# Performance work log

Hardware: AMD Instinct MI355X
Metric: run time of the kernel (lower is better)

The kernel has to match this reference:

```python
import jax, jax.numpy as jnp
import numpy as np

N_EMBED = 1024
EMBED_DIM = 64
BETA = 0.25


def setup_inputs() -> dict:
    key = jax.random.key(0)
    k1, k2 = jax.random.split(key)
    z = jax.random.normal(k1, (16, EMBED_DIM, 64, 64), dtype=jnp.float32)
    # torch init: uniform(-1/n_embed, 1/n_embed)
    embed_weight = jax.random.uniform(
        k2, (N_EMBED, EMBED_DIM), dtype=jnp.float32,
        minval=-1.0 / N_EMBED, maxval=1.0 / N_EMBED)
    return {"z": z, "embed_weight": embed_weight}


def reference(z, embed_weight):
    # z: (B, C, H, W) with C == embed_dim
    n_embed = embed_weight.shape[0]
    zp = jnp.transpose(z, (0, 2, 3, 1))                     # (B,H,W,C)
    zf = zp.reshape(-1, zp.shape[-1])                       # (N,C)
    # squared euclidean distances: ||z||^2 - 2 z.e + ||e||^2
    dist = (jnp.sum(zf * zf, axis=1, keepdims=True)
            - 2.0 * (zf @ embed_weight.T)
            + jnp.sum(embed_weight * embed_weight, axis=1))  # (N,n_embed)
    embed_index = jnp.argmin(dist, axis=1)                  # (N,)
    embed_onehot = jax.nn.one_hot(embed_index, n_embed, dtype=zf.dtype)
    # one-hot @ codebook is just a gather
    quantize = embed_weight[embed_index].reshape(zp.shape)  # (B,H,W,C)
    vq_loss = (jnp.mean((jax.lax.stop_gradient(quantize) - zp) ** 2)
               + BETA * jnp.mean((quantize - jax.lax.stop_gradient(zp)) ** 2))
    # straight-through estimator
    quantize_st = zp + jax.lax.stop_gradient(quantize - zp)
    e_mean = jnp.mean(embed_onehot, axis=0)
    perplexity = jnp.exp(-jnp.sum(e_mean * jnp.log(e_mean + 1e-10)))
    quantize_out = jnp.transpose(quantize_st, (0, 3, 1, 2))  # (B,C,H,W)
    return (quantize_out, vq_loss, perplexity, embed_onehot, embed_index)
```

## Files before the change

### kernel.cpp

```cpp
#include <hip/hip_runtime.h>
#include <math.h>


#define HW 4096
#define OUT_Q    0ull
#define OUT_LOSS 4194304ull
#define OUT_PERP 4194305ull
#define OUT_OH   4194306ull
#define OUT_IDX  71303170ull

typedef float f32x16 __attribute__((ext_vector_type(16)));

__global__ void vq_setup(const float* __restrict__ W,
                         float* __restrict__ wsf, int* __restrict__ wsi) {
    const int b = blockIdx.x, tid = threadIdx.x;
    if (tid < 64) wsi[b * 64 + tid] = 0;
    if (b == 0 && tid == 0) wsf[1024] = 0.0f;
    const int wave = tid >> 6, lane = tid & 63;
    for (int p = 0; p < 16; ++p) {
        const int code = b * 64 + p * 4 + wave;
        const float a = W[code * 64 + lane];
        const float sq = __fmul_rn(a, a);
        float t = sq;
        #pragma unroll
        for (int m = 1; m < 8; ++m) t = __fadd_rn(t, __shfl(sq, lane + 8 * m, 64));
        const float u  = __fadd_rn(t, __shfl_xor(t, 1, 64));
        const float v  = __fadd_rn(u, __shfl_xor(u, 2, 64));
        const float w2 = __fadd_rn(v, __shfl_xor(v, 4, 64));
        if (lane == 0) wsf[1028 + code] = w2;
    }
}

__global__ __launch_bounds__(256, 2)
void vq_main(const float* __restrict__ Z, const float* __restrict__ W,
             float* __restrict__ out, float* __restrict__ wsf, int* __restrict__ wsi) {
    __shared__ __align__(16) float qT[64 * 65];
    __shared__ __align__(16) float ldsC[1024];
    __shared__ float cand_v[256];
    __shared__ int   cand_i[256];
    __shared__ int   mi[64];

    const int tid  = threadIdx.x;
    const int wave = tid >> 6;
    const int lane = tid & 63;
    const int blk  = blockIdx.x;
    const int b    = blk >> 6;
    const int hw0  = (blk & 63) << 6;
    const int rowbase = b * HW + hw0;

    ((float4*)ldsC)[tid] = ((const float4*)(wsf + 1028))[tid];

    const float* zb = Z + (size_t)b * 64 * HW + hw0 + lane;
    float zr[64];
    #pragma unroll
    for (int c = 0; c < 64; ++c) zr[c] = zb[(size_t)c * HW];

    float r[8];
    #pragma unroll
    for (int j = 0; j < 8; ++j) r[j] = __fmul_rn(zr[j], zr[j]);
    #pragma unroll
    for (int i = 8; i < 64; i += 8) {
        #pragma unroll
        for (int j = 0; j < 8; ++j) r[j] = __fadd_rn(r[j], __fmul_rn(zr[i + j], zr[i + j]));
    }
    const float A = __fadd_rn(__fadd_rn(__fadd_rn(r[0], r[1]), __fadd_rn(r[2], r[3])),
                              __fadd_rn(__fadd_rn(r[4], r[5]), __fadd_rn(r[6], r[7])));

    __syncthreads();

    const float* Wwave = (const float*)((const char*)W +
                         __builtin_amdgcn_readfirstlane(wave << 8));

    float bestv = __builtin_huge_valf();
    int   besti = 0;

    for (int i = 0; i < 256; ++i) {
        const int code = i * 4 + wave;
        const float* wrow = (const float*)((const char*)Wwave + (i << 10));
        f32x16 a0, a1, a2, a3;
        asm volatile(
            "s_load_dwordx16 %0, %4, 0x0\n\t"
            "s_load_dwordx16 %1, %4, 0x40\n\t"
            "s_load_dwordx16 %2, %4, 0x80\n\t"
            "s_load_dwordx16 %3, %4, 0xc0\n\t"
            "s_waitcnt lgkmcnt(0)"
            : "=&s"(a0), "=&s"(a1), "=&s"(a2), "=&s"(a3)
            : "s"(wrow));
        float dot = 0.0f;
        #pragma unroll
        for (int k = 0; k < 16; ++k) dot = __fmaf_rn(zr[k],      a0[k], dot);
        #pragma unroll
        for (int k = 0; k < 16; ++k) dot = __fmaf_rn(zr[16 + k], a1[k], dot);
        #pragma unroll
        for (int k = 0; k < 16; ++k) dot = __fmaf_rn(zr[32 + k], a2[k], dot);
        #pragma unroll
        for (int k = 0; k < 16; ++k) dot = __fmaf_rn(zr[48 + k], a3[k], dot);
        const float d = __fadd_rn(__fsub_rn(A, 2.0f * dot), ldsC[code]);
        if (d < bestv) { bestv = d; besti = code; }
    }

    cand_v[wave * 64 + lane] = bestv;
    cand_i[wave * 64 + lane] = besti;
    __syncthreads();
    if (wave == 0) {
        float bv = cand_v[lane]; int bi = cand_i[lane];
        #pragma unroll
        for (int s = 1; s < 4; ++s) {
            const float v  = cand_v[s * 64 + lane];
            const int   i2 = cand_i[s * 64 + lane];
            if (v < bv || (v == bv && i2 < bi)) { bv = v; bi = i2; }
        }
        mi[lane] = bi;
        out[OUT_IDX + rowbase + lane] = (float)bi;
        atomicAdd(&wsi[bi], 1);
    }
    __syncthreads();

    {
        const int m = mi[lane];
        const float4* wq = (const float4*)(W + m * 64);
        #pragma unroll
        for (int j4 = 0; j4 < 4; ++j4) {
            const float4 q = wq[wave * 4 + j4];
            const int c0 = wave * 16 + j4 * 4;
            qT[lane * 65 + c0 + 0] = q.x;
            qT[lane * 65 + c0 + 1] = q.y;
            qT[lane * 65 + c0 + 2] = q.z;
            qT[lane * 65 + c0 + 3] = q.w;
        }
    }
    __syncthreads();

    float lsum = 0.0f;
    #pragma unroll
    for (int j = 0; j < 16; ++j) {
        const int c = j * 4 + wave;
        const float qv = qT[lane * 65 + c];
        const float zv = zr[c];
        const float dd = __fsub_rn(qv, zv);
        lsum = __fmaf_rn(dd, dd, lsum);
        out[OUT_Q + (size_t)(b * 64 + c) * HW + hw0 + lane] = __fadd_rn(zv, dd);
    }
    #pragma unroll
    for (int s = 32; s > 0; s >>= 1) lsum += __shfl_xor(lsum, s, 64);
    if (lane == 0) atomicAdd(wsf + 1024, lsum);

    for (int i = 0; i < 64; ++i) {
        const int m = mi[i];
        float* basep = out + OUT_OH + (size_t)(rowbase + i) * 1024;
        const int c0 = tid * 2;
        float2 v0, v1;
        v0.x = (c0       == m) ? 1.0f : 0.0f;
        v0.y = (c0 + 1   == m) ? 1.0f : 0.0f;
        v1.x = (c0 + 512 == m) ? 1.0f : 0.0f;
        v1.y = (c0 + 513 == m) ? 1.0f : 0.0f;
        *(float2*)(basep + c0)       = v0;
        *(float2*)(basep + 512 + c0) = v1;
    }
}

__global__ void vq_final(const int* __restrict__ wsi, const float* __restrict__ wsf,
                         float* __restrict__ out) {
    __shared__ double red[256];
    const int tid = threadIdx.x;
    double s = 0.0;
    for (int j = tid; j < 1024; j += 256) {
        const float e  = (float)wsi[j] * (1.0f / 65536.0f);
        const float lg = logf(__fadd_rn(e, 1e-10f));
        s += (double)__fmul_rn(e, lg);
    }
    red[tid] = s;
    __syncthreads();
    for (int st = 128; st > 0; st >>= 1) {
        if (tid < st) red[tid] += red[tid + st];
        __syncthreads();
    }
    if (tid == 0) {
        out[OUT_PERP] = expf((float)(-red[0]));
        const float ms = wsf[1024] * (1.0f / 4194304.0f);
        out[OUT_LOSS] = __fadd_rn(ms, __fmul_rn(0.25f, ms));
    }
}

extern "C" void kernel_launch(void* const* d_in, const int* in_sizes, int n_in,
                              void* d_out, int out_size, void* d_ws, size_t ws_size,
                              hipStream_t stream) {
    const float* Z = (const float*)d_in[0];
    const float* W = (const float*)d_in[1];
    float* out = (float*)d_out;
    float* wsf = (float*)d_ws;
    int*   wsi = (int*)d_ws;
    vq_setup<<<16,   256, 0, stream>>>(W, wsf, wsi);
    vq_main <<<1024, 256, 0, stream>>>(Z, W, out, wsf, wsi);
    vq_final<<<1,    256, 0, stream>>>(wsi, wsf, out);
}
```

Measured before the change: 461.4 us.

## Split VQ kernel into codebook-halved distance pass and separate output pass

The fused main kernel is split in two. A distance kernel launches twice as many blocks, each scanning half of the codebook, and writes per-row best candidates to workspace. A separate output kernel merges the two halves, rereads Z, and writes the quantized values, indices and one-hot rows. This doubles parallelism in the compute-heavy argmin phase and decouples the store-heavy one-hot writes from its register pressure, at the cost of an extra launch plus re-reading Z and the candidates.

```diff
diff --git a/kernel.cpp b/kernel.cpp
--- a/kernel.cpp
+++ b/kernel.cpp
@@ -8,6 +8,7 @@
 #define OUT_PERP 4194305ull
 #define OUT_OH   4194306ull
 #define OUT_IDX  71303170ull
+#define WS_CAND  2052
 
 typedef float f32x16 __attribute__((ext_vector_type(16)));
 
@@ -31,22 +32,22 @@
     }
 }
 
-__global__ __launch_bounds__(256, 2)
-void vq_main(const float* __restrict__ Z, const float* __restrict__ W,
-             float* __restrict__ out, float* __restrict__ wsf, int* __restrict__ wsi) {
-    __shared__ __align__(16) float qT[64 * 65];
+__global__ __launch_bounds__(256)
+void vq_dist(const float* __restrict__ Z, const float* __restrict__ W,
+             float* __restrict__ wsf) {
     __shared__ __align__(16) float ldsC[1024];
     __shared__ float cand_v[256];
     __shared__ int   cand_i[256];
-    __shared__ int   mi[64];
 
     const int tid  = threadIdx.x;
     const int wave = tid >> 6;
     const int lane = tid & 63;
     const int blk  = blockIdx.x;
-    const int b    = blk >> 6;
-    const int hw0  = (blk & 63) << 6;
-    const int rowbase = b * HW + hw0;
+    const int half = blk & 1;
+    const int rblk = blk >> 1;
+    const int b    = rblk >> 6;
+    const int hw0  = (rblk & 63) << 6;
+    const int rowbase = rblk << 6;
 
     ((float4*)ldsC)[tid] = ((const float4*)(wsf + 1028))[tid];
 
@@ -69,13 +70,13 @@
     __syncthreads();
 
     const float* Wwave = (const float*)((const char*)W +
-                         __builtin_amdgcn_readfirstlane(wave << 8));
+                         __builtin_amdgcn_readfirstlane((half << 17) + (wave << 8)));
 
     float bestv = __builtin_huge_valf();
     int   besti = 0;
 
-    for (int i = 0; i < 256; ++i) {
-        const int code = i * 4 + wave;
+    for (int i = 0; i < 128; ++i) {
+        const int code = half * 512 + i * 4 + wave;
         const float* wrow = (const float*)((const char*)Wwave + (i << 10));
         f32x16 a0, a1, a2, a3;
         asm volatile(
@@ -110,6 +111,31 @@
             const int   i2 = cand_i[s * 64 + lane];
             if (v < bv || (v == bv && i2 < bi)) { bv = v; bi = i2; }
         }
+        const int row = rowbase + lane;
+        float2 pk; pk.x = bv; pk.y = __int_as_float(bi);
+        *(float2*)(wsf + WS_CAND + row * 4 + half * 2) = pk;
+    }
+}
+
+__global__ __launch_bounds__(256)
+void vq_out(const float* __restrict__ Z, const float* __restrict__ W,
+            float* __restrict__ out, float* __restrict__ wsf, int* __restrict__ wsi) {
+    __shared__ __align__(16) float qT[64 * 65];
+    __shared__ int mi[64];
+
+    const int tid  = threadIdx.x;
+    const int wave = tid >> 6;
+    const int lane = tid & 63;
+    const int rblk = blockIdx.x;
+    const int b    = rblk >> 6;
+    const int hw0  = (rblk & 63) << 6;
+    const int rowbase = rblk << 6;
+
+    if (wave == 0) {
+        const float4 c4 = *(const float4*)(wsf + WS_CAND + (rowbase + lane) * 4);
+        const float v0 = c4.x, v1 = c4.z;
+        const int   i0 = __float_as_int(c4.y), i1 = __float_as_int(c4.w);
+        const int bi = (v1 < v0) ? i1 : i0;
         mi[lane] = bi;
         out[OUT_IDX + rowbase + lane] = (float)bi;
         atomicAdd(&wsi[bi], 1);
@@ -136,7 +162,7 @@
     for (int j = 0; j < 16; ++j) {
         const int c = j * 4 + wave;
         const float qv = qT[lane * 65 + c];
-        const float zv = zr[c];
+        const float zv = Z[(size_t)(b * 64 + c) * HW + hw0 + lane];
         const float dd = __fsub_rn(qv, zv);
         lsum = __fmaf_rn(dd, dd, lsum);
         out[OUT_Q + (size_t)(b * 64 + c) * HW + hw0 + lane] = __fadd_rn(zv, dd);
@@ -191,6 +217,7 @@
     float* wsf = (float*)d_ws;
     int*   wsi = (int*)d_ws;
     vq_setup<<<16,   256, 0, stream>>>(W, wsf, wsi);
-    vq_main <<<1024, 256, 0, stream>>>(Z, W, out, wsf, wsi);
+    vq_dist <<<2048, 256, 0, stream>>>(Z, W, wsf);
+    vq_out  <<<1024, 256, 0, stream>>>(Z, W, out, wsf, wsi);
     vq_final<<<1,    256, 0, stream>>>(wsi, wsf, out);
 }
```

Measured after the change: 482.6 us. 1.05x slower.
